# Optimization experiments

Hardware: AMD Instinct MI355X
Metric: run time of the kernel (lower is better)

## Reference

```python
import jax, jax.numpy as jnp
import numpy as np

# ---- static config (matches init_kwargs) ----
N, E = 8192, 262144
IN_CH, MP_CH, HID, K = 128, 512, 256, 10
EPS, DELTA = 1e-3, 0.311
TV_COEFF, BAL_COEFF = 0.785, 0.514


def setup_inputs() -> dict:
    key = jax.random.key(0)
    ks = jax.random.split(key, 16)

    def p(k, shape):
        fan_in = shape[0] if len(shape) > 1 else shape[0]
        return (jax.random.normal(k, shape, jnp.float32) / np.sqrt(fan_in)).astype(jnp.float32)

    return {
        "x": jax.random.normal(ks[0], (N, IN_CH), jnp.float32),
        "edge_index": jax.random.randint(ks[1], (2, E), 0, N, jnp.int32),
        "edge_weight": jax.random.uniform(ks[2], (E,), jnp.float32),
        # GTVConv layer 1 / 2 (Linear weight + bias)
        "W1": p(ks[3], (IN_CH, MP_CH)), "b1": jnp.zeros((MP_CH,), jnp.float32),
        "W2": p(ks[4], (MP_CH, MP_CH)), "b2": jnp.zeros((MP_CH,), jnp.float32),
        # pooling MLP [512 -> 256 -> K], relu, no norm
        "Wm1": p(ks[5], (MP_CH, HID)), "bm1": jnp.zeros((HID,), jnp.float32),
        "Wm2": p(ks[6], (HID, K)), "bm2": jnp.zeros((K,), jnp.float32),
    }


def _gtv_conv(x, src, dst, w, W, b):
    """GTVConv: out = elu( h - delta*(D_G h - Gamma h) + b ),
    gamma_ij = w_ij / max(||h_i - h_j||_1, eps), h = x @ W."""
    h = x @ W                                   # [N, C]
    diff = jnp.sum(jnp.abs(h[src] - h[dst]), axis=-1)   # [E]
    gamma = w / jnp.maximum(diff, EPS)                  # [E]
    deg = jnp.zeros(h.shape[0], h.dtype).at[dst].add(gamma)          # [N]
    agg = jnp.zeros_like(h).at[dst].add(gamma[:, None] * h[src])     # Gamma @ h
    out = h - DELTA * (deg[:, None] * h - agg) + b
    return jax.nn.elu(out)


def reference(x, edge_index, edge_weight, W1, b1, W2, b2, Wm1, bm1, Wm2, bm2):
    src, dst = edge_index[0], edge_index[1]

    h = _gtv_conv(x, src, dst, edge_weight, W1, b1)
    h = _gtv_conv(h, src, dst, edge_weight, W2, b2)

    # pooling MLP -> cluster logits s
    s_logits = jax.nn.relu(h @ Wm1 + bm1) @ Wm2 + bm2   # [N, K]

    # dense adjacency (to_dense_adj: duplicate edges accumulate)
    adj = jnp.zeros((N, N), x.dtype).at[src, dst].add(edge_weight)

    s = jax.nn.softmax(s_logits, axis=-1)

    # total-variation loss: sum_ij a_ij * sum_k |s_ik - s_jk| / (2 * nnz(adj))
    tv = jnp.zeros((), x.dtype)
    for k in range(K):  # small fixed loop over clusters, avoids [N,N,K] tensor
        col = s[:, k]
        tv = tv + jnp.sum(adj * jnp.abs(col[:, None] - col[None, :]))
    n_edges = jax.lax.stop_gradient(jnp.count_nonzero(adj).astype(x.dtype))
    tv = tv / (2.0 * n_edges)

    # asymmetric-norm balance loss (AsymCheegerCut)
    idx = N // K + 1                         # rho-quantile index (static)
    quant = jnp.sort(s, axis=0)[N - idx]     # idx-th largest per cluster, [K]
    t = s - quant[None, :]
    asym = jnp.where(t >= 0, (K - 1) * t, -t)
    denom = float(N * (K - 1))
    bal = (denom - jnp.sum(asym)) / denom

    return s_logits, TV_COEFF * tv, BAL_COEFF * bal
```

## Files before the change

kernel.cpp:

```cpp
#include <hip/hip_runtime.h>

#define N_NODES 8192
#define N_EDGES 262144
#define IN_CH 128
#define MP_CH 512
#define HID 256
#define KCL 10
#define EPS_C 0.001f
#define DELTA_C 0.311f
#define TV_COEFF_C 0.785f
#define BAL_COEFF_C 0.514f
#define RANK1 7373

typedef __bf16 bf16x8 __attribute__((ext_vector_type(8)));
typedef float f32x4 __attribute__((ext_vector_type(4)));
typedef unsigned short ushort8 __attribute__((ext_vector_type(8)));

__device__ __forceinline__ float bf2f(unsigned short h) {
  union { unsigned int u; float f; } c; c.u = ((unsigned int)h) << 16; return c.f;
}
__device__ __forceinline__ unsigned short f2bf(float f) {
  union { float f; unsigned int u; } c; c.f = f;
  unsigned int r = c.u + 0x7fffu + ((c.u >> 16) & 1u);
  return (unsigned short)(r >> 16);
}

__global__ void prep_kernel(const float* __restrict__ x, const float* __restrict__ W1,
                            const float* __restrict__ W2, const float* __restrict__ Wm1,
                            unsigned short* __restrict__ xb, unsigned short* __restrict__ W1bt,
                            unsigned short* __restrict__ W2bt, unsigned short* __restrict__ Wm1bt,
                            const int* __restrict__ dst, int* __restrict__ cnt) {
  int i = blockIdx.x * 256 + threadIdx.x;
  if (i < 1048576) { xb[i] = f2bf(x[i]); return; }
  i -= 1048576;
  if (i < 65536) { int n = i >> 7, k = i & 127; W1bt[i] = f2bf(W1[k * MP_CH + n]); return; }
  i -= 65536;
  if (i < 262144) { int n = i >> 9, k = i & 511; W2bt[i] = f2bf(W2[k * MP_CH + n]); return; }
  i -= 262144;
  if (i < 131072) { int n = i >> 9, k = i & 511; Wm1bt[i] = f2bf(Wm1[k * HID + n]); return; }
  i -= 131072;
  if (i < N_EDGES) atomicAdd(&cnt[dst[i]], 1);
}

__global__ __launch_bounds__(1024) void scan_kernel(const int* __restrict__ cnt,
                                                    int* __restrict__ offs,
                                                    int* __restrict__ cursor) {
  __shared__ int ts[1024];
  int t = threadIdx.x;
  int v[8]; int s = 0;
#pragma unroll
  for (int j = 0; j < 8; ++j) { v[j] = cnt[t * 8 + j]; s += v[j]; }
  ts[t] = s; __syncthreads();
  for (int off = 1; off < 1024; off <<= 1) {
    int add = (t >= off) ? ts[t - off] : 0;
    __syncthreads();
    ts[t] += add;
    __syncthreads();
  }
  int base = ts[t] - s;
#pragma unroll
  for (int j = 0; j < 8; ++j) { offs[t * 8 + j] = base; cursor[t * 8 + j] = base; base += v[j]; }
  if (t == 1023) offs[N_NODES] = ts[1023];
}

__global__ void fill_kernel(const int* __restrict__ src, const int* __restrict__ dst,
                            const float* __restrict__ ew, int* __restrict__ cursor,
                            int2* __restrict__ esw) {
  for (int e = blockIdx.x * blockDim.x + threadIdx.x; e < N_EDGES; e += gridDim.x * blockDim.x) {
    int p = atomicAdd(&cursor[dst[e]], 1);
    esw[p] = make_int2(src[e], __float_as_int(ew[e]));
  }
}

__global__ __launch_bounds__(256) void gemm_bt(
    const unsigned short* __restrict__ A, const unsigned short* __restrict__ BT,
    float* __restrict__ C, unsigned short* __restrict__ Cb,
    const float* __restrict__ bias, int N, int K, int epi) {
  __shared__ unsigned short lA[128 * 32];
  __shared__ unsigned short lB[128 * 32];
  int lane = threadIdx.x & 63;
  int wv = threadIdx.x >> 6;
  int tm = blockIdx.y * 128, tn = blockIdx.x * 128;
  int wm = (wv >> 1) * 64, wn = (wv & 1) * 64;
  int rA = lane & 15, quad = lane >> 4;
  f32x4 acc[4][4];
#pragma unroll
  for (int i = 0; i < 4; ++i)
#pragma unroll
    for (int j = 0; j < 4; ++j) acc[i][j] = (f32x4){0.f, 0.f, 0.f, 0.f};

  int arow = wv * 32 + (lane >> 2);
  int acol = (lane & 3) * 8;

  for (int k0 = 0; k0 < K; k0 += 32) {
#pragma unroll
    for (int c = 0; c < 2; ++c) {
      const unsigned short* ga = A + (size_t)(tm + arow + c * 16) * K + k0 + acol;
      __builtin_amdgcn_global_load_lds(
          (const __attribute__((address_space(1))) unsigned int*)ga,
          (__attribute__((address_space(3))) unsigned int*)(lA + (wv * 32 + c * 16) * 32),
          16, 0, 0);
      const unsigned short* gb = BT + (size_t)(tn + arow + c * 16) * K + k0 + acol;
      __builtin_amdgcn_global_load_lds(
          (const __attribute__((address_space(1))) unsigned int*)gb,
          (__attribute__((address_space(3))) unsigned int*)(lB + (wv * 32 + c * 16) * 32),
          16, 0, 0);
    }
    __syncthreads();
    bf16x8 af[4], bfr[4];
#pragma unroll
    for (int i = 0; i < 4; ++i)
      af[i] = *(const bf16x8*)(lA + (wm + i * 16 + rA) * 32 + quad * 8);
#pragma unroll
    for (int j = 0; j < 4; ++j)
      bfr[j] = *(const bf16x8*)(lB + (wn + j * 16 + rA) * 32 + quad * 8);
#pragma unroll
    for (int i = 0; i < 4; ++i)
#pragma unroll
      for (int j = 0; j < 4; ++j)
        acc[i][j] = __builtin_amdgcn_mfma_f32_16x16x32_bf16(af[i], bfr[j], acc[i][j], 0, 0, 0);
    __syncthreads();
  }

#pragma unroll
  for (int i = 0; i < 4; ++i)
#pragma unroll
    for (int j = 0; j < 4; ++j)
#pragma unroll
      for (int r = 0; r < 4; ++r) {
        int row = tm + wm + i * 16 + quad * 4 + r;
        int col = tn + wn + j * 16 + rA;
        float v = acc[i][j][r];
        size_t idx = (size_t)row * N + col;
        if (epi == 1) { v += bias[col]; v = fmaxf(v, 0.f); C[idx] = v; }
        else { C[idx] = v; Cb[idx] = f2bf(v); }
      }
}

__global__ __launch_bounds__(256, 8) void gtv_node(
    const unsigned short* __restrict__ hb, const float* __restrict__ hf,
    const float* __restrict__ bias, const int2* __restrict__ esw,
    const int* __restrict__ offs, unsigned short* __restrict__ outb) {
  int lane = threadIdx.x & 63;
  int wv = threadIdx.x >> 6;
  int d = __builtin_amdgcn_readfirstlane(blockIdx.x * 4 + wv);
  ushort8 hdv = ((const ushort8*)(hb + (size_t)d * MP_CH))[lane];
  float hd[8], acc[8];
#pragma unroll
  for (int j = 0; j < 8; ++j) { hd[j] = bf2f(hdv[j]); acc[j] = 0.f; }
  int e0 = offs[d], e1 = offs[d + 1];
  int i = e0;
  for (; i + 1 < e1; i += 2) {
    int2 ma = esw[i], mb = esw[i + 1];
    float wa = __int_as_float(ma.y), wb = __int_as_float(mb.y);
    ushort8 va = ((const ushort8*)(hb + (size_t)ma.x * MP_CH))[lane];
    ushort8 vb = ((const ushort8*)(hb + (size_t)mb.x * MP_CH))[lane];
    float pa = 0.f, pb = 0.f;
#pragma unroll
    for (int j = 0; j < 8; ++j) {
      pa += fabsf(hd[j] - bf2f(va[j]));
      pb += fabsf(hd[j] - bf2f(vb[j]));
    }
#pragma unroll
    for (int m = 1; m < 64; m <<= 1) { pa += __shfl_xor(pa, m, 64); pb += __shfl_xor(pb, m, 64); }
    float ga = wa * __builtin_amdgcn_rcpf(fmaxf(pa, EPS_C));
    float gb = wb * __builtin_amdgcn_rcpf(fmaxf(pb, EPS_C));
#pragma unroll
    for (int j = 0; j < 8; ++j)
      acc[j] += ga * (hd[j] - bf2f(va[j])) + gb * (hd[j] - bf2f(vb[j]));
  }
  if (i < e1) {
    int2 m0 = esw[i];
    float w = __int_as_float(m0.y);
    ushort8 sv = ((const ushort8*)(hb + (size_t)m0.x * MP_CH))[lane];
    float part = 0.f;
#pragma unroll
    for (int j = 0; j < 8; ++j) part += fabsf(hd[j] - bf2f(sv[j]));
#pragma unroll
    for (int m = 1; m < 64; m <<= 1) part += __shfl_xor(part, m, 64);
    float g = w * __builtin_amdgcn_rcpf(fmaxf(part, EPS_C));
#pragma unroll
    for (int j = 0; j < 8; ++j) acc[j] += g * (hd[j] - bf2f(sv[j]));
  }
  const f32x4* hfr = (const f32x4*)(hf + (size_t)d * MP_CH + lane * 8);
  const f32x4* br  = (const f32x4*)(bias + lane * 8);
  f32x4 h0 = hfr[0], h1 = hfr[1];
  f32x4 b0 = br[0], b1 = br[1];
  unsigned short ov[8];
#pragma unroll
  for (int j = 0; j < 8; ++j) {
    float hfv = (j < 4) ? h0[j] : h1[j - 4];
    float bv  = (j < 4) ? b0[j] : b1[j - 4];
    float o = hfv - DELTA_C * acc[j] + bv;
    o = (o > 0.f) ? o : (expf(o) - 1.f);
    ov[j] = f2bf(o);
  }
  *((ushort8*)(outb + (size_t)d * MP_CH) + lane) = *(ushort8*)ov;
}

__global__ __launch_bounds__(256) void gemm_small(
    const float* __restrict__ hm, const float* __restrict__ W,
    const float* __restrict__ b, float* __restrict__ out, float* __restrict__ s) {
  __shared__ float lw[HID * KCL];
  __shared__ float lb[KCL];
  for (int i = threadIdx.x; i < HID * KCL; i += 256) lw[i] = W[i];
  if (threadIdx.x < KCL) lb[threadIdx.x] = b[threadIdx.x];
  __syncthreads();
  int lane = threadIdx.x & 63, wv = threadIdx.x >> 6;
  int row = blockIdx.x * 4 + wv;
  f32x4 hv = *(const f32x4*)(hm + (size_t)row * HID + lane * 4);
  float p[KCL];
#pragma unroll
  for (int n = 0; n < KCL; ++n) {
    int k0 = lane * 4;
    p[n] = hv[0] * lw[(k0 + 0) * KCL + n] + hv[1] * lw[(k0 + 1) * KCL + n] +
           hv[2] * lw[(k0 + 2) * KCL + n] + hv[3] * lw[(k0 + 3) * KCL + n];
  }
#pragma unroll
  for (int n = 0; n < KCL; ++n)
#pragma unroll
    for (int m = 1; m < 64; m <<= 1) p[n] += __shfl_xor(p[n], m, 64);
  if (lane == 0) {
    float vv[KCL]; float mx = -1e30f;
#pragma unroll
    for (int n = 0; n < KCL; ++n) {
      vv[n] = p[n] + lb[n];
      out[(size_t)row * KCL + n] = vv[n];
      mx = fmaxf(mx, vv[n]);
    }
    float sum = 0.f;
#pragma unroll
    for (int n = 0; n < KCL; ++n) { vv[n] = expf(vv[n] - mx); sum += vv[n]; }
    float inv = 1.f / sum;
#pragma unroll
    for (int n = 0; n < KCL; ++n) s[(size_t)row * KCL + n] = vv[n] * inv;
  }
}

__global__ __launch_bounds__(256) void tv_kernel(
    const int* __restrict__ src, const int* __restrict__ dst,
    const float* __restrict__ ew, const float* __restrict__ s,
    unsigned int* __restrict__ bitmap, float* __restrict__ tv_sum) {
  float local = 0.f;
  for (int e = blockIdx.x * blockDim.x + threadIdx.x; e < N_EDGES; e += gridDim.x * blockDim.x) {
    int a = src[e], b = dst[e];
    float w = ew[e];
    const float* sa = s + (size_t)a * KCL;
    const float* sb = s + (size_t)b * KCL;
    float t = 0.f;
#pragma unroll
    for (int k = 0; k < KCL; ++k) t += fabsf(sa[k] - sb[k]);
    local += w * t;
    if (w != 0.f) {
      unsigned int key = ((unsigned int)a << 13) | (unsigned int)b;
      atomicOr(&bitmap[key >> 5], 1u << (key & 31u));
    }
  }
#pragma unroll
  for (int m = 1; m < 64; m <<= 1) local += __shfl_xor(local, m, 64);
  __shared__ float wsum[4];
  int lane = threadIdx.x & 63, wv = threadIdx.x >> 6;
  if (lane == 0) wsum[wv] = local;
  __syncthreads();
  if (threadIdx.x == 0) atomicAdd(tv_sum, wsum[0] + wsum[1] + wsum[2] + wsum[3]);
}

__global__ __launch_bounds__(256) void popc_kernel(const unsigned int* __restrict__ bm,
                                                   int* __restrict__ cnt) {
  int local = 0;
  for (int i = blockIdx.x * blockDim.x + threadIdx.x; i < (1 << 21); i += gridDim.x * blockDim.x)
    local += __popc(bm[i]);
#pragma unroll
  for (int m = 1; m < 64; m <<= 1) local += __shfl_xor(local, m, 64);
  __shared__ int wsum[4];
  int lane = threadIdx.x & 63, wv = threadIdx.x >> 6;
  if (lane == 0) wsum[wv] = local;
  __syncthreads();
  if (threadIdx.x == 0) atomicAdd(cnt, wsum[0] + wsum[1] + wsum[2] + wsum[3]);
}

__global__ __launch_bounds__(1024) void quant_kernel(const float* __restrict__ s,
                                                     float* __restrict__ asym_sum) {
  __shared__ int wcnt[16];
  __shared__ float fsum[16];
  __shared__ unsigned int bounds[2];
  int k = blockIdx.x, t = threadIdx.x;
  int lane = t & 63, wv = t >> 6;
  unsigned int v[8];
#pragma unroll
  for (int j = 0; j < 8; ++j)
    v[j] = __float_as_uint(s[(size_t)(t + j * 1024) * KCL + k]);
  if (t == 0) { bounds[0] = 0u; bounds[1] = 0x3F800000u; }
  __syncthreads();
  unsigned int lo = bounds[0], hi = bounds[1];
  while (lo < hi) {
    unsigned int mid = (lo + hi) >> 1;
    int c = 0;
#pragma unroll
    for (int j = 0; j < 8; ++j) c += (v[j] <= mid) ? 1 : 0;
#pragma unroll
    for (int m = 1; m < 64; m <<= 1) c += __shfl_xor(c, m, 64);
    if (lane == 0) wcnt[wv] = c;
    __syncthreads();
    if (t == 0) {
      int tot = 0;
#pragma unroll
      for (int i2 = 0; i2 < 16; ++i2) tot += wcnt[i2];
      if (tot >= RANK1) bounds[1] = mid; else bounds[0] = mid + 1;
    }
    __syncthreads();
    lo = bounds[0]; hi = bounds[1];
  }
  float q = __uint_as_float(lo);
  float local = 0.f;
#pragma unroll
  for (int j = 0; j < 8; ++j) {
    float tt = __uint_as_float(v[j]) - q;
    local += (tt >= 0.f) ? 9.f * tt : -tt;
  }
#pragma unroll
  for (int m = 1; m < 64; m <<= 1) local += __shfl_xor(local, m, 64);
  if (lane == 0) fsum[wv] = local;
  __syncthreads();
  if (t == 0) {
    float tot = 0.f;
#pragma unroll
    for (int i2 = 0; i2 < 16; ++i2) tot += fsum[i2];
    atomicAdd(asym_sum, tot);
  }
}

__global__ void finalize_kernel(const float* __restrict__ scal, const int* __restrict__ ne,
                                float* __restrict__ out) {
  if (threadIdx.x == 0) {
    float tv = scal[0], asym = scal[1];
    float nedges = (float)(*ne);
    out[N_NODES * KCL] = TV_COEFF_C * (tv / (2.f * nedges));
    out[N_NODES * KCL + 1] = BAL_COEFF_C * ((73728.f - asym) / 73728.f);
  }
}

#define OFF_H      ((size_t)0)
#define OFF_HB     ((size_t)16777216)
#define OFF_OUTB   ((size_t)25165824)
#define OFF_HM     ((size_t)33554432)
#define OFF_XB     ((size_t)41943040)
#define OFF_W1BT   ((size_t)44040192)
#define OFF_W2BT   ((size_t)44171264)
#define OFF_WM1BT  ((size_t)44695552)
#define OFF_S      ((size_t)44957696)
#define OFF_CNT    ((size_t)45285376)
#define OFF_OFFS   ((size_t)45318144)
#define OFF_CURSOR ((size_t)45351168)
#define OFF_SCAL   ((size_t)46432512)

extern "C" void kernel_launch(void* const* d_in, const int* in_sizes, int n_in,
                              void* d_out, int out_size, void* d_ws, size_t ws_size,
                              hipStream_t stream) {
  const float* x   = (const float*)d_in[0];
  const int*   ei  = (const int*)d_in[1];
  const float* ew  = (const float*)d_in[2];
  const float* W1  = (const float*)d_in[3];
  const float* b1  = (const float*)d_in[4];
  const float* W2  = (const float*)d_in[5];
  const float* b2  = (const float*)d_in[6];
  const float* Wm1 = (const float*)d_in[7];
  const float* bm1 = (const float*)d_in[8];
  const float* Wm2 = (const float*)d_in[9];
  const float* bm2 = (const float*)d_in[10];
  float* out = (float*)d_out;

  char* ws = (char*)d_ws;
  float*          h      = (float*)(ws + OFF_H);
  unsigned int*   bitmap = (unsigned int*)(ws + OFF_H);
  unsigned short* hb     = (unsigned short*)(ws + OFF_HB);
  unsigned short* outb   = (unsigned short*)(ws + OFF_OUTB);
  float*          hm     = (float*)(ws + OFF_HM);
  int2*           esw    = (int2*)(ws + OFF_HM);
  unsigned short* xb     = (unsigned short*)(ws + OFF_XB);
  unsigned short* W1bt   = (unsigned short*)(ws + OFF_W1BT);
  unsigned short* W2bt   = (unsigned short*)(ws + OFF_W2BT);
  unsigned short* Wm1bt  = (unsigned short*)(ws + OFF_WM1BT);
  float*          s      = (float*)(ws + OFF_S);
  int*            cnt    = (int*)(ws + OFF_CNT);
  int*            offs   = (int*)(ws + OFF_OFFS);
  int*            cursor = (int*)(ws + OFF_CURSOR);
  float*          scal   = (float*)(ws + OFF_SCAL);
  int*            nep    = (int*)(scal + 2);

  const int* srcA = ei;
  const int* dstA = ei + N_EDGES;

  hipMemsetAsync(cnt, 0, N_NODES * sizeof(int), stream);
  hipMemsetAsync(scal, 0, 64, stream);

  prep_kernel<<<6912, 256, 0, stream>>>(x, W1, W2, Wm1, xb, W1bt, W2bt, Wm1bt, dstA, cnt);
  scan_kernel<<<1, 1024, 0, stream>>>(cnt, offs, cursor);
  fill_kernel<<<1024, 256, 0, stream>>>(srcA, dstA, ew, cursor, esw);

  gemm_bt<<<dim3(MP_CH / 128, N_NODES / 128), 256, 0, stream>>>(
      xb, W1bt, h, hb, nullptr, MP_CH, IN_CH, 0);
  gtv_node<<<N_NODES / 4, 256, 0, stream>>>(hb, h, b1, esw, offs, outb);
  gemm_bt<<<dim3(MP_CH / 128, N_NODES / 128), 256, 0, stream>>>(
      outb, W2bt, h, hb, nullptr, MP_CH, MP_CH, 0);
  gtv_node<<<N_NODES / 4, 256, 0, stream>>>(hb, h, b2, esw, offs, outb);
  gemm_bt<<<dim3(HID / 128, N_NODES / 128), 256, 0, stream>>>(
      outb, Wm1bt, hm, nullptr, bm1, HID, MP_CH, 1);
  gemm_small<<<N_NODES / 4, 256, 0, stream>>>(hm, Wm2, bm2, out, s);

  hipMemsetAsync(bitmap, 0, (size_t)1 << 23, stream);
  tv_kernel<<<1024, 256, 0, stream>>>(srcA, dstA, ew, s, bitmap, scal);
  popc_kernel<<<1024, 256, 0, stream>>>(bitmap, nep);
  quant_kernel<<<KCL, 1024, 0, stream>>>(s, scal + 1);
  finalize_kernel<<<1, 64, 0, stream>>>(scal, nep, out);
}
```

Before: 308.6 us.

## Software-prefetch neighbor rows in GTV node loop; halve barriers in quantile search

```diff
diff --git a/kernel.cpp b/kernel.cpp
--- a/kernel.cpp
+++ b/kernel.cpp
@@ -149,38 +149,45 @@
 #pragma unroll
   for (int j = 0; j < 8; ++j) { hd[j] = bf2f(hdv[j]); acc[j] = 0.f; }
   int e0 = offs[d], e1 = offs[d + 1];
-  int i = e0;
-  for (; i + 1 < e1; i += 2) {
-    int2 ma = esw[i], mb = esw[i + 1];
-    float wa = __int_as_float(ma.y), wb = __int_as_float(mb.y);
+  if (e0 < e1) {
+    int last = e1 - 1;
+    int2 ma = esw[e0];
+    int2 mb = esw[(e0 + 1 <= last) ? e0 + 1 : last];
+    float wa = __int_as_float(ma.y);
+    float wb = (e0 + 1 <= last) ? __int_as_float(mb.y) : 0.f;
     ushort8 va = ((const ushort8*)(hb + (size_t)ma.x * MP_CH))[lane];
     ushort8 vb = ((const ushort8*)(hb + (size_t)mb.x * MP_CH))[lane];
-    float pa = 0.f, pb = 0.f;
-#pragma unroll
-    for (int j = 0; j < 8; ++j) {
-      pa += fabsf(hd[j] - bf2f(va[j]));
-      pb += fabsf(hd[j] - bf2f(vb[j]));
+    for (int i = e0;;) {
+      int ni = i + 2;
+      bool more = ni <= last;
+      int2 mc, md; ushort8 vc, vd; float wc = 0.f, wd = 0.f;
+      if (more) {
+        mc = esw[ni];
+        md = esw[(ni + 1 <= last) ? ni + 1 : last];
+        wc = __int_as_float(mc.y);
+        wd = (ni + 1 <= last) ? __int_as_float(md.y) : 0.f;
+        vc = ((const ushort8*)(hb + (size_t)mc.x * MP_CH))[lane];
+        vd = ((const ushort8*)(hb + (size_t)md.x * MP_CH))[lane];
+      }
+      float pa = 0.f, pb = 0.f;
+#pragma unroll
+      for (int j = 0; j < 8; ++j) {
+        pa += fabsf(hd[j] - bf2f(va[j]));
+        pb += fabsf(hd[j] - bf2f(vb[j]));
+      }
+#pragma unroll
+      for (int m = 1; m < 64; m <<= 1) {
+        pa += __shfl_xor(pa, m, 64);
+        pb += __shfl_xor(pb, m, 64);
+      }
+      float ga = wa * __builtin_amdgcn_rcpf(fmaxf(pa, EPS_C));
+      float gb = wb * __builtin_amdgcn_rcpf(fmaxf(pb, EPS_C));
+#pragma unroll
+      for (int j = 0; j < 8; ++j)
+        acc[j] += ga * (hd[j] - bf2f(va[j])) + gb * (hd[j] - bf2f(vb[j]));
+      if (!more) break;
+      va = vc; vb = vd; wa = wc; wb = wd; i = ni;
     }
-#pragma unroll
-    for (int m = 1; m < 64; m <<= 1) { pa += __shfl_xor(pa, m, 64); pb += __shfl_xor(pb, m, 64); }
-    float ga = wa * __builtin_amdgcn_rcpf(fmaxf(pa, EPS_C));
-    float gb = wb * __builtin_amdgcn_rcpf(fmaxf(pb, EPS_C));
-#pragma unroll
-    for (int j = 0; j < 8; ++j)
-      acc[j] += ga * (hd[j] - bf2f(va[j])) + gb * (hd[j] - bf2f(vb[j]));
-  }
-  if (i < e1) {
-    int2 m0 = esw[i];
-    float w = __int_as_float(m0.y);
-    ushort8 sv = ((const ushort8*)(hb + (size_t)m0.x * MP_CH))[lane];
-    float part = 0.f;
-#pragma unroll
-    for (int j = 0; j < 8; ++j) part += fabsf(hd[j] - bf2f(sv[j]));
-#pragma unroll
-    for (int m = 1; m < 64; m <<= 1) part += __shfl_xor(part, m, 64);
-    float g = w * __builtin_amdgcn_rcpf(fmaxf(part, EPS_C));
-#pragma unroll
-    for (int j = 0; j < 8; ++j) acc[j] += g * (hd[j] - bf2f(sv[j]));
   }
   const f32x4* hfr = (const f32x4*)(hf + (size_t)d * MP_CH + lane * 8);
   const f32x4* br  = (const f32x4*)(bias + lane * 8);
@@ -281,18 +288,16 @@
 
 __global__ __launch_bounds__(1024) void quant_kernel(const float* __restrict__ s,
                                                      float* __restrict__ asym_sum) {
-  __shared__ int wcnt[16];
+  __shared__ int wcnt[2][16];
   __shared__ float fsum[16];
-  __shared__ unsigned int bounds[2];
   int k = blockIdx.x, t = threadIdx.x;
   int lane = t & 63, wv = t >> 6;
   unsigned int v[8];
 #pragma unroll
   for (int j = 0; j < 8; ++j)
     v[j] = __float_as_uint(s[(size_t)(t + j * 1024) * KCL + k]);
-  if (t == 0) { bounds[0] = 0u; bounds[1] = 0x3F800000u; }
-  __syncthreads();
-  unsigned int lo = bounds[0], hi = bounds[1];
+  unsigned int lo = 0u, hi = 0x3F800000u;
+  int p = 0;
   while (lo < hi) {
     unsigned int mid = (lo + hi) >> 1;
     int c = 0;
@@ -300,16 +305,13 @@
     for (int j = 0; j < 8; ++j) c += (v[j] <= mid) ? 1 : 0;
 #pragma unroll
     for (int m = 1; m < 64; m <<= 1) c += __shfl_xor(c, m, 64);
-    if (lane == 0) wcnt[wv] = c;
+    if (lane == 0) wcnt[p][wv] = c;
     __syncthreads();
-    if (t == 0) {
-      int tot = 0;
-#pragma unroll
-      for (int i2 = 0; i2 < 16; ++i2) tot += wcnt[i2];
-      if (tot >= RANK1) bounds[1] = mid; else bounds[0] = mid + 1;
-    }
-    __syncthreads();
-    lo = bounds[0]; hi = bounds[1];
+    int tot = 0;
+#pragma unroll
+    for (int i2 = 0; i2 < 16; ++i2) tot += wcnt[p][i2];
+    if (tot >= RANK1) hi = mid; else lo = mid + 1;
+    p ^= 1;
   }
   float q = __uint_as_float(lo);
   float local = 0.f;
```

Result: slower. 314.8 us (+2.0%).
